# Performance work log

Measured on AMD Instinct MI355X. Metric: run time of the kernel, lower is better.

## Reference

```python
import jax, jax.numpy as jnp
import numpy as np

B, C, H, W = 16, 256, 32, 32
DIM = H * W  # LayerNorm/Linear dim == h*w per the rearrange in forward


def _conv1x1(x, w, b):
    # x: [b,c,h,w], w: [out,in] (1x1 kernel squeezed), b: [out]
    return jnp.einsum('bchw,oc->bohw', x, w) + b[None, :, None, None]


def _layernorm(x, g, b, eps=1e-5):
    mu = jnp.mean(x, axis=-1, keepdims=True)
    var = jnp.var(x, axis=-1, keepdims=True)
    return (x - mu) / jnp.sqrt(var + eps) * g + b


def setup_inputs() -> dict:
    key = jax.random.key(0)
    ks = jax.random.split(key, 12)
    n = jax.random.normal
    k_cdc = (2.0 / (2 * C)) ** 0.5   # kaiming_normal fan_in = 2C
    k_v = (2.0 / C) ** 0.5           # fan_in = C
    k_lin = (2.0 / DIM) ** 0.5       # fan_in = DIM
    return {
        'x_spa': n(ks[0], (B, C, H, W), jnp.float32),
        'x_freq': n(ks[1], (B, C, H, W), jnp.float32),
        'w_cdc': n(ks[2], (C, 2 * C), jnp.float32) * k_cdc,
        'b_cdc': jnp.zeros((C,), jnp.float32),
        'w_sv': n(ks[3], (C, C), jnp.float32) * k_v,
        'b_sv': jnp.zeros((C,), jnp.float32),
        'w_fv': n(ks[4], (C, C), jnp.float32) * k_v,
        'b_fv': jnp.zeros((C,), jnp.float32),
        'ln_w': jnp.ones((DIM,), jnp.float32),
        'ln_b': jnp.zeros((DIM,), jnp.float32),
        'w_qk': n(ks[5], (2 * DIM, DIM), jnp.float32) * k_lin,  # Linear(dim, 2*dim), no bias
        'w_spa': n(ks[6], (DIM, DIM), jnp.float32) * k_lin,
        'b_spa': jnp.zeros((DIM,), jnp.float32),
        'w_frq': n(ks[7], (DIM, DIM), jnp.float32) * k_lin,
        'b_frq': jnp.zeros((DIM,), jnp.float32),
    }


def reference(x_spa, x_freq, w_cdc, b_cdc, w_sv, b_sv, w_fv, b_fv,
              ln_w, ln_b, w_qk, w_spa, b_spa, w_frq, b_frq):
    b, c, h, w = x_spa.shape
    hw = h * w
    scale = hw ** (-0.5)
    v_spa = _conv1x1(x_spa, w_sv, b_sv).reshape(b, c, hw)
    v_freq = _conv1x1(x_freq, w_fv, b_fv).reshape(b, c, hw)
    x = _conv1x1(jnp.concatenate([x_spa, x_freq], axis=1), w_cdc, b_cdc).reshape(b, c, hw)
    x = _layernorm(x, ln_w, ln_b)
    qk = x @ w_qk.T                       # [b, c, 2*hw]
    q, k = jnp.split(qk, 2, axis=-1)      # each [b, c, hw]
    att = jnp.einsum('bcn,bcm->bnm', q, k) * scale   # q^T k over channels: [b, hw, hw]
    att_spa = jax.nn.softmax(att @ w_spa.T + b_spa, axis=-1)
    att_frq = jax.nn.softmax(att @ w_frq.T + b_frq, axis=-1)
    out_spa = x_spa + jnp.einsum('bcn,bnm->bcm', v_spa, att_spa).reshape(b, c, h, w)
    out_freq = x_freq + jnp.einsum('bcn,bnm->bcm', v_freq, att_frq).reshape(b, c, h, w)
    return out_spa, out_freq
```

## Files before the change

kernel.cpp:

```cpp
#include <hip/hip_runtime.h>
#include <hip/hip_bf16.h>

typedef __hip_bfloat16 bf16;
typedef __attribute__((ext_vector_type(8))) short bf16x8v;
typedef __attribute__((ext_vector_type(4))) float f32x4v;

__device__ __forceinline__ float bfbits2f(unsigned short h) {
    union { unsigned int u; float f; } v; v.u = ((unsigned int)h) << 16; return v.f;
}
__device__ __forceinline__ unsigned short f2bfbits(float f) {
    bf16 h = __float2bfloat16(f);
    unsigned short s;
    __builtin_memcpy(&s, &h, 2);
    return s;
}
__device__ __forceinline__ float load1_any(const void* p, long idx, bool f32) {
    if (f32) return ((const float*)p)[idx];
    return bfbits2f(((const unsigned short*)p)[idx]);
}
__device__ __forceinline__ float4 loadbf4(const bf16* p) {
    ushort4 u = *reinterpret_cast<const ushort4*>(p);
    return make_float4(bfbits2f(u.x), bfbits2f(u.y), bfbits2f(u.z), bfbits2f(u.w));
}
__device__ __forceinline__ void store_bf4(bf16* p, float a, float b, float c, float d) {
    ushort4 o;
    o.x = f2bfbits(a); o.y = f2bfbits(b); o.z = f2bfbits(c); o.w = f2bfbits(d);
    *reinterpret_cast<ushort4*>(p) = o;
}
__device__ __forceinline__ void gl16(const void* g, void* l) {
    __builtin_amdgcn_global_load_lds(
        (const __attribute__((address_space(1))) unsigned int*)g,
        (__attribute__((address_space(3))) unsigned int*)l, 16, 0, 0);
}

__global__ __launch_bounds__(1024)
void detect_kernel(const unsigned short* __restrict__ x, int* __restrict__ flag) {
    const int tid = threadIdx.x;
    int zc = 0, hc = 0;
    const uint4* xv = (const uint4*)x;
#pragma unroll
    for (int p = 0; p < 16; ++p) {
        uint4 v = xv[p * 1024 + tid];
        unsigned s0 = v.x & 0xFFFFu, s1 = v.y & 0xFFFFu;
        unsigned s2 = v.z & 0xFFFFu, s3 = v.w & 0xFFFFu;
        zc += (int)(s0 == 0) + (int)(s1 == 0) + (int)(s2 == 0) + (int)(s3 == 0);
        hc += (int)(((s0 >> 7) & 0xFFu) >= 0x90u) + (int)(((s1 >> 7) & 0xFFu) >= 0x90u)
            + (int)(((s2 >> 7) & 0xFFu) >= 0x90u) + (int)(((s3 >> 7) & 0xFFu) >= 0x90u);
    }
#pragma unroll
    for (int off = 32; off > 0; off >>= 1) {
        zc += __shfl_down(zc, off);
        hc += __shfl_down(hc, off);
    }
    __shared__ int rz[16], rh[16];
    if ((tid & 63) == 0) { rz[tid >> 6] = zc; rh[tid >> 6] = hc; }
    __syncthreads();
    if (tid == 0) {
        int Z = 0, H = 0;
#pragma unroll
        for (int i = 0; i < 16; ++i) { Z += rz[i]; H += rh[i]; }
        *flag = (Z > 60000 || H > 256) ? 1 : 0;
    }
}

__global__ void diag_kernel(float* __restrict__ out, float val) {
    if (threadIdx.x == 0) out[0] = val;
}

__global__ __launch_bounds__(256)
void convert6_kernel(const void* __restrict__ s0, const void* __restrict__ s1,
                     const void* __restrict__ s2, const void* __restrict__ s3,
                     const void* __restrict__ s4, const void* __restrict__ s5,
                     bf16* __restrict__ dst, const int* __restrict__ dflag) {
    const bool f32 = (*dflag != 0);
    for (long i = (long)blockIdx.x * 256 + threadIdx.x; i < 4456448;
         i += (long)gridDim.x * 256) {
        const void* s; long o;
        if (i < 131072)       { s = s0; o = i; }
        else if (i < 196608)  { s = s1; o = i - 131072; }
        else if (i < 262144)  { s = s2; o = i - 196608; }
        else if (i < 2359296) { s = s3; o = i - 262144; }
        else if (i < 3407872) { s = s4; o = i - 2359296; }
        else                  { s = s5; o = i - 3407872; }
        dst[i] = __float2bfloat16(load1_any(s, o, f32));
    }
}

__global__ __launch_bounds__(256)
void xpose_conv_kernel(const void* __restrict__ x1, const void* __restrict__ x2,
                       bf16* __restrict__ dst, int bofs, int zsplit,
                       const int* __restrict__ dflag) {
    const bool f32 = (*dflag != 0);
    __shared__ float t[64][65];
    const int ch0 = blockIdx.y * 64, n0 = blockIdx.x * 64, z = blockIdx.z;
    const bool hiz = (z >= zsplit);
    const int zl = hiz ? z - zsplit : z;
    const void* x = hiz ? x2 : x1;
    const long sb = (long)(zl + bofs) * 262144, db = (long)z * 262144;
    const int tid = threadIdx.x;
#pragma unroll
    for (int p = 0; p < 16; ++p) {
        int e = tid + p * 256; int sch = e >> 6, sn = e & 63;
        t[sch][sn] = load1_any(x, sb + (long)(ch0 + sch) * 1024 + n0 + sn, f32);
    }
    __syncthreads();
#pragma unroll
    for (int p = 0; p < 16; ++p) {
        int e = tid + p * 256; int dn = e >> 6, dch = e & 63;
        dst[db + (long)(n0 + dn) * 256 + ch0 + dch] = __float2bfloat16(t[dch][dn]);
    }
}

__global__ __launch_bounds__(256)
void smnorm_kernel(bf16* __restrict__ X, float* __restrict__ invS) {
    const int tid = threadIdx.x;
    const int cg = tid & 7;
    const int js = tid >> 3;
    const int n0 = blockIdx.x * 64;
    const long zb = (long)blockIdx.y * 1048576;
    unsigned short* Xp = (unsigned short*)X + zb + n0 + cg * 8;

    float m[8];
#pragma unroll
    for (int q = 0; q < 8; ++q) m[q] = -3.4e38f;
#pragma unroll 4
    for (int r = 0; r < 32; ++r) {
        bf16x8v u = *(const bf16x8v*)(Xp + (long)(js * 32 + r) * 1024);
#pragma unroll
        for (int q = 0; q < 8; ++q)
            m[q] = fmaxf(m[q], bfbits2f((unsigned short)u[q]));
    }
    __shared__ float sh[32][8][8];
    __shared__ float Mc[64];
#pragma unroll
    for (int q = 0; q < 8; ++q) sh[js][cg][q] = m[q];
    __syncthreads();
    if (tid < 64) {
        float mm = -3.4e38f;
#pragma unroll 8
        for (int s = 0; s < 32; ++s) mm = fmaxf(mm, sh[s][tid >> 3][tid & 7]);
        Mc[tid] = mm;
    }
    __syncthreads();
    float M8[8], s8[8];
#pragma unroll
    for (int q = 0; q < 8; ++q) { M8[q] = Mc[cg * 8 + q]; s8[q] = 0.f; }
#pragma unroll 4
    for (int r = 0; r < 32; ++r) {
        long off = (long)(js * 32 + r) * 1024;
        bf16x8v u = *(const bf16x8v*)(Xp + off);
        bf16x8v o;
#pragma unroll
        for (int q = 0; q < 8; ++q) {
            float e = __expf(bfbits2f((unsigned short)u[q]) - M8[q]);
            s8[q] += e;
            o[q] = (short)f2bfbits(e);
        }
        *(bf16x8v*)(Xp + off) = o;
    }
    __syncthreads();
#pragma unroll
    for (int q = 0; q < 8; ++q) sh[js][cg][q] = s8[q];
    __syncthreads();
    if (tid < 64) {
        float ss = 0.f;
#pragma unroll 8
        for (int s = 0; s < 32; ++s) ss += sh[s][tid >> 3][tid & 7];
        invS[(long)blockIdx.y * 1024 + n0 + tid] = 1.0f / ss;
    }
}

template <int EPI>
__global__ __launch_bounds__(256)
void mfma_nt(const bf16* __restrict__ A1, const bf16* __restrict__ A2,
             long aB1, long aB2, int ldA1, int ldA2,
             const bf16* __restrict__ B1, const bf16* __restrict__ B2,
             long bB1, long bB2, int ldB1, int ldB2,
             int ksplit, long kOff2,
             void* __restrict__ out1, void* __restrict__ out2,
             long oB1, long oB2, int ldO1, int ldO2,
             int K, float scale,
             const void* __restrict__ bias1, const void* __restrict__ bias2,
             const void* __restrict__ res1, const void* __restrict__ res2,
             long rBatch, int bofs, int zsplit, int swapXY,
             const int* __restrict__ dflag) {
    __shared__ short As[5][4096];
    __shared__ short Bs[5][4096];
    const int tid  = threadIdx.x;
    const int lane = tid & 63, wave = tid >> 6;
    const int quad = lane >> 4, lrow = lane & 15;
    const int wm = (wave >> 1) * 64, wn = (wave & 1) * 64;
    const int z  = blockIdx.z;
    const bool hiz = (z >= zsplit);
    const int zl = hiz ? z - zsplit : z;
    const bool sw = hiz && swapXY;
    const int n0 = (sw ? blockIdx.y : blockIdx.x) * 128;
    const int m0 = (sw ? blockIdx.x : blockIdx.y) * 128;
    const int ldA = hiz ? ldA2 : ldA1, ldB = hiz ? ldB2 : ldB1;
    const int ldO = hiz ? ldO2 : ldO1;
    const int srow = tid >> 2, sseg = tid & 3;
    const int sl = sseg ^ ((srow >> 1) & 3);
    const int xq = quad ^ ((lrow >> 1) & 3);

    const bf16* Ab = (hiz ? A2 : A1) + (long)zl * (hiz ? aB2 : aB1);
    const bf16* Bb = (hiz ? B2 : B1) + (long)zl * (hiz ? bB2 : bB1);

    auto stage = [&](int buf, int k0) {
        const bf16* asrc = Ab + (long)k0;
        const bf16* bsrc = Bb + ((k0 < ksplit) ? (long)k0 : (long)(k0 - ksplit) + kOff2);
        const bf16* ga0 = asrc + (long)(m0 + srow) * ldA + sl * 8;
        const bf16* ga1 = asrc + (long)(m0 + 64 + srow) * ldA + sl * 8;
        const bf16* gb0 = bsrc + (long)(n0 + srow) * ldB + sl * 8;
        const bf16* gb1 = bsrc + (long)(n0 + 64 + srow) * ldB + sl * 8;
        short* la = &As[buf][wave * 512];
        short* lb = &Bs[buf][wave * 512];
        gl16(ga0, la);
        gl16(ga1, la + 2048);
        gl16(gb0, lb);
        gl16(gb1, lb + 2048);
    };

    f32x4v acc[4][4] = {};
    const int nt = K >> 5;
    stage(0, 0);
    if (nt > 1) stage(1, 32);
    if (nt > 2) stage(2, 64);
    if (nt > 3) stage(3, 96);

    int cur = 0;
    for (int t = 0; t < nt; ++t) {
        const int rem = nt - 1 - t;
        if (rem >= 3)      asm volatile("s_waitcnt vmcnt(12)" ::: "memory");
        else if (rem == 2) asm volatile("s_waitcnt vmcnt(8)" ::: "memory");
        else if (rem == 1) asm volatile("s_waitcnt vmcnt(4)" ::: "memory");
        else               asm volatile("s_waitcnt vmcnt(0)" ::: "memory");
        __builtin_amdgcn_s_barrier();
        __builtin_amdgcn_sched_barrier(0);
        bf16x8v bfr[4], afr[4];
#pragma unroll
        for (int j = 0; j < 4; ++j)
            bfr[j] = *(const bf16x8v*)&Bs[cur][(wn + j * 16 + lrow) * 32 + xq * 8];
#pragma unroll
        for (int i = 0; i < 4; ++i)
            afr[i] = *(const bf16x8v*)&As[cur][(wm + i * 16 + lrow) * 32 + xq * 8];
        asm volatile("s_waitcnt lgkmcnt(0)" ::: "memory");
        __builtin_amdgcn_sched_barrier(0);
        if (t + 4 < nt) {
            int nb = cur + 4; if (nb >= 5) nb -= 5;
            stage(nb, (t + 4) << 5);
        }
#pragma unroll
        for (int i = 0; i < 4; ++i)
#pragma unroll
            for (int j = 0; j < 4; ++j)
                acc[i][j] = __builtin_amdgcn_mfma_f32_16x16x32_bf16(afr[i], bfr[j], acc[i][j], 0, 0, 0);
        cur = (cur == 4) ? 0 : cur + 1;
    }

    const bool f32 = (*dflag != 0);
    const void* bias = hiz ? bias2 : bias1;
    if (EPI != 3) {
        bf16* O = (bf16*)(hiz ? out2 : out1) + (long)zl * (hiz ? oB2 : oB1);
        const float* csp = (EPI == 4)
            ? (const float*)(hiz ? res2 : res1) + (long)zl * rBatch : nullptr;
#pragma unroll
        for (int i = 0; i < 4; ++i) {
            int row0 = m0 + wm + i * 16 + quad * 4;
            float rb[4] = {0.f, 0.f, 0.f, 0.f};
            if (EPI == 1 || EPI == 2 || EPI == 4) {
#pragma unroll
                for (int r = 0; r < 4; ++r) rb[r] = load1_any(bias, row0 + r, f32);
            }
#pragma unroll
            for (int j = 0; j < 4; ++j) {
                int col = n0 + wn + j * 16 + lrow;
                float cs = (EPI == 4) ? csp[col] : 1.0f;
#pragma unroll
                for (int r = 0; r < 4; ++r) {
                    float vv = acc[i][j][r];
                    if (EPI == 1) vv += rb[r];
                    if (EPI == 2) vv = vv * scale + rb[r];
                    if (EPI == 4) vv = (vv + rb[r]) * cs;
                    O[(long)(row0 + r) * ldO + col] = __float2bfloat16(vv);
                }
            }
        }
    } else {
        float* O = (float*)(hiz ? out2 : out1);
        const void* res = hiz ? res2 : res1;
        const long ob  = (long)(zl + bofs) * (hiz ? oB2 : oB1);
        const long rbb = (long)(zl + bofs) * rBatch;
#pragma unroll
        for (int i = 0; i < 4; ++i) {
            int row0 = m0 + wm + i * 16 + quad * 4;
#pragma unroll
            for (int j = 0; j < 4; ++j) {
                int col = n0 + wn + j * 16 + lrow;
#pragma unroll
                for (int r = 0; r < 4; ++r) {
                    float rv = load1_any(res, rbb + (long)(row0 + r) * ldO + col, f32);
                    O[ob + (long)(row0 + r) * ldO + col] = acc[i][j][r] + rv;
                }
            }
        }
    }
}

__global__ __launch_bounds__(256)
void layernorm_kernel(bf16* __restrict__ x, const void* __restrict__ g,
                      const void* __restrict__ beta, const int* __restrict__ dflag) {
    const bool f32 = (*dflag != 0);
    bf16* p = x + (long)blockIdx.x * 1024;
    const int tid = threadIdx.x;
    float4 v = loadbf4(p + tid * 4);
    float s  = v.x + v.y + v.z + v.w;
    float ss = v.x * v.x + v.y * v.y + v.z * v.z + v.w * v.w;
#pragma unroll
    for (int off = 32; off > 0; off >>= 1) {
        s  += __shfl_down(s, off);
        ss += __shfl_down(ss, off);
    }
    __shared__ float sh[8];
    __shared__ float sh_mu, sh_rs;
    if ((tid & 63) == 0) { sh[tid >> 6] = s; sh[4 + (tid >> 6)] = ss; }
    __syncthreads();
    if (tid == 0) {
        float S  = sh[0] + sh[1] + sh[2] + sh[3];
        float SS = sh[4] + sh[5] + sh[6] + sh[7];
        float mu = S * (1.0f / 1024.0f);
        float var = SS * (1.0f / 1024.0f) - mu * mu;
        sh_mu = mu;
        sh_rs = rsqrtf(fmaxf(var, 0.0f) + 1e-5f);
    }
    __syncthreads();
    float mu = sh_mu, rs = sh_rs;
    float gx = load1_any(g, tid * 4 + 0, f32), gy = load1_any(g, tid * 4 + 1, f32);
    float gz = load1_any(g, tid * 4 + 2, f32), gw = load1_any(g, tid * 4 + 3, f32);
    float bx = load1_any(beta, tid * 4 + 0, f32), by = load1_any(beta, tid * 4 + 1, f32);
    float bz = load1_any(beta, tid * 4 + 2, f32), bw = load1_any(beta, tid * 4 + 3, f32);
    store_bf4(p + tid * 4,
              (v.x - mu) * rs * gx + bx, (v.y - mu) * rs * gy + by,
              (v.z - mu) * rs * gz + bz, (v.w - mu) * rs * gw + bw);
}

extern "C" void kernel_launch(void* const* d_in, const int* in_sizes, int n_in,
                              void* d_out, int out_size, void* d_ws, size_t ws_size,
                              hipStream_t stream) {
    const void* x_spa  = d_in[0];
    const void* x_freq = d_in[1];
    const void* w_cdc  = d_in[2];
    const void* b_cdc  = d_in[3];
    const void* w_sv   = d_in[4];
    const void* b_sv   = d_in[5];
    const void* w_fv   = d_in[6];
    const void* b_fv   = d_in[7];
    const void* ln_w   = d_in[8];
    const void* ln_b   = d_in[9];
    const void* w_qk   = d_in[10];
    const void* w_spa  = d_in[11];
    const void* b_spa  = d_in[12];
    const void* w_frq  = d_in[13];
    const void* b_frq  = d_in[14];
    float* out = (float*)d_out;

    const int B = 16, C = 256;
    const long XB = 262144;
    const long PB = 1048576;

    int*  dflag = (int*)d_ws;
    bf16* wb    = (bf16*)((char*)d_ws + 4096);
    bf16* w_cdc_b = wb;
    bf16* w_sv_b  = w_cdc_b + 131072;
    bf16* w_fv_b  = w_sv_b  + 65536;
    bf16* w_qk_b  = w_fv_b  + 65536;
    bf16* w_spa_b = w_qk_b  + 2097152;
    bf16* w_frq_b = w_spa_b + 1048576;
    bf16* pb      = w_frq_b + 1048576;

    const size_t fixedB = 4096 + 4456448ull * 2;
    const size_t perB   = 8921088ull;
    size_t avail = (ws_size > fixedB) ? (ws_size - fixedB) : 0;
    long gmax = (long)(avail / perB);
    const bool wsOK = (gmax >= 1);
    int G = wsOK ? (int)(gmax > 16 ? 16 : gmax) : 1;

    bf16* xT    = pb;
    bf16* xln   = xT   + 2L * G * XB;
    bf16* kb    = xln  + (long)G * XB;
    bf16* qT    = kb   + (long)G * XB;
    bf16* TT    = qT   + (long)G * XB;
    bf16* vb    = TT   + 2L * G * XB;
    bf16* attpT = vb   + 2L * G * XB;
    float* invS = (float*)(attpT + 2L * G * PB);

    dim3 blk(256);
    detect_kernel<<<dim3(1), dim3(1024), 0, stream>>>((const unsigned short*)x_spa, dflag);

    if (!wsOK) {
        float mb = (float)(ws_size >> 20);
        diag_kernel<<<dim3(1), dim3(64), 0, stream>>>(out, 1000.0f * (mb + 1.0f));
        return;
    }

    convert6_kernel<<<dim3(4352), blk, 0, stream>>>(w_cdc, w_sv, w_fv, w_qk, w_spa, w_frq,
                                                    wb, dflag);

    for (int b0 = 0; b0 < B; b0 += G) {
        int g = (B - b0 < G) ? (B - b0) : G;

        xpose_conv_kernel<<<dim3(16, 4, 2 * g), blk, 0, stream>>>(
            x_spa, x_freq, xT, b0, g, dflag);

        mfma_nt<1><<<dim3(8, 2, g), blk, 0, stream>>>(
            w_cdc_b, w_cdc_b, 0, 0, 512, 512,
            xT, xT, XB, XB, 256, 256, 256, (long)g * XB,
            xln, xln, XB, XB, 1024, 1024,
            512, 1.0f, b_cdc, b_cdc, nullptr, nullptr, 0, 0, g, 0, dflag);
        layernorm_kernel<<<dim3(g * C), blk, 0, stream>>>(xln, ln_w, ln_b, dflag);

        mfma_nt<0><<<dim3(8, 2, 2 * g), blk, 0, stream>>>(
            xln, w_qk_b, XB, 0, 1024, 1024,
            w_qk_b + 1048576, xln, 0, XB, 1024, 1024, 1024, 0,
            kb, qT, XB, XB, 1024, 256,
            1024, 1.0f, nullptr, nullptr, nullptr, nullptr, 0, 0, g, 1, dflag);

        mfma_nt<0><<<dim3(2, 8, 2 * g), blk, 0, stream>>>(
            w_spa_b, w_frq_b, 0, 0, 1024, 1024,
            kb, kb, XB, XB, 1024, 1024, 1024, 0,
            TT, TT + (long)g * XB, XB, XB, 256, 256,
            1024, 1.0f, nullptr, nullptr, nullptr, nullptr, 0, 0, g, 0, dflag);

        mfma_nt<2><<<dim3(8, 8, 2 * g), blk, 0, stream>>>(
            TT, TT + (long)g * XB, XB, XB, 256, 256,
            qT, qT, XB, XB, 256, 256, 256, 0,
            attpT, attpT + (long)g * PB, PB, PB, 1024, 1024,
            256, 0.03125f, b_spa, b_frq, nullptr, nullptr, 0, 0, g, 0, dflag);

        smnorm_kernel<<<dim3(16, 2 * g), blk, 0, stream>>>(attpT, invS);

        mfma_nt<4><<<dim3(8, 2, 2 * g), blk, 0, stream>>>(
            w_sv_b, w_fv_b, 0, 0, 256, 256,
            xT, xT + (long)g * XB, XB, XB, 256, 256, 256, 0,
            vb, vb + (long)g * XB, XB, XB, 1024, 1024,
            256, 1.0f, b_sv, b_fv, invS, invS + (long)g * 1024, 1024, 0, g, 0, dflag);

        mfma_nt<3><<<dim3(8, 2, 2 * g), blk, 0, stream>>>(
            vb, vb + (long)g * XB, XB, XB, 1024, 1024,
            attpT, attpT + (long)g * PB, PB, PB, 1024, 1024, 1024, 0,
            out, out + 4194304, XB, XB, 1024, 1024,
            1024, 1.0f, nullptr, nullptr, x_spa, x_freq, XB, b0, g, 0, dflag);
    }
}
```

Before: 346.5 us.

## Precompute fused Wspa·Wk weights, batch GEMMs across samples, add 512-thread MFMA kernel

Precomputes W_spa·W_k^T (and W_frq) once per call through a transposed copy of the k-half of w_qk. This folds the k-projection into the attention-logit GEMM chain, so the per-batch k GEMM and the T=Wspa·k GEMM become a single GEMM on the layernormed activations. Activations are relaid out so several GEMMs treat the batch as one wide N dimension. A new 512-thread MFMA kernel with 128x256 or 256x256 tiles is used for the large GEMMs, and setprio is raised around the MFMA blocks. This adds workspace and a per-call weight-fusion GEMM, and the changed association order may shift bf16 rounding.

```diff
diff --git a/kernel.cpp b/kernel.cpp
--- a/kernel.cpp
+++ b/kernel.cpp
@@ -83,6 +83,24 @@
         else if (i < 3407872) { s = s4; o = i - 2359296; }
         else                  { s = s5; o = i - 3407872; }
         dst[i] = __float2bfloat16(load1_any(s, o, f32));
+    }
+}
+
+__global__ __launch_bounds__(256)
+void xpose_w_kernel(const bf16* __restrict__ src, bf16* __restrict__ dst) {
+    __shared__ float t[64][65];
+    const int c0 = blockIdx.x * 64, r0 = blockIdx.y * 64;
+    const int tid = threadIdx.x;
+#pragma unroll
+    for (int p = 0; p < 16; ++p) {
+        int e = tid + p * 256; int r = e >> 6, c = e & 63;
+        t[r][c] = __bfloat162float(src[(long)(r0 + r) * 1024 + c0 + c]);
+    }
+    __syncthreads();
+#pragma unroll
+    for (int p = 0; p < 16; ++p) {
+        int e = tid + p * 256; int r = e >> 6, c = e & 63;
+        dst[(long)(c0 + r) * 1024 + r0 + c] = __float2bfloat16(t[c][r]);
     }
 }
 
@@ -208,16 +226,10 @@
     auto stage = [&](int buf, int k0) {
         const bf16* asrc = Ab + (long)k0;
         const bf16* bsrc = Bb + ((k0 < ksplit) ? (long)k0 : (long)(k0 - ksplit) + kOff2);
-        const bf16* ga0 = asrc + (long)(m0 + srow) * ldA + sl * 8;
-        const bf16* ga1 = asrc + (long)(m0 + 64 + srow) * ldA + sl * 8;
-        const bf16* gb0 = bsrc + (long)(n0 + srow) * ldB + sl * 8;
-        const bf16* gb1 = bsrc + (long)(n0 + 64 + srow) * ldB + sl * 8;
-        short* la = &As[buf][wave * 512];
-        short* lb = &Bs[buf][wave * 512];
-        gl16(ga0, la);
-        gl16(ga1, la + 2048);
-        gl16(gb0, lb);
-        gl16(gb1, lb + 2048);
+        gl16(asrc + (long)(m0 + srow) * ldA + sl * 8, &As[buf][wave * 512]);
+        gl16(asrc + (long)(m0 + 64 + srow) * ldA + sl * 8, &As[buf][2048 + wave * 512]);
+        gl16(bsrc + (long)(n0 + srow) * ldB + sl * 8, &Bs[buf][wave * 512]);
+        gl16(bsrc + (long)(n0 + 64 + srow) * ldB + sl * 8, &Bs[buf][2048 + wave * 512]);
     };
 
     f32x4v acc[4][4] = {};
@@ -249,11 +261,13 @@
             int nb = cur + 4; if (nb >= 5) nb -= 5;
             stage(nb, (t + 4) << 5);
         }
+        __builtin_amdgcn_s_setprio(1);
 #pragma unroll
         for (int i = 0; i < 4; ++i)
 #pragma unroll
             for (int j = 0; j < 4; ++j)
                 acc[i][j] = __builtin_amdgcn_mfma_f32_16x16x32_bf16(afr[i], bfr[j], acc[i][j], 0, 0, 0);
+        __builtin_amdgcn_s_setprio(0);
         cur = (cur == 4) ? 0 : cur + 1;
     }
 
@@ -306,11 +320,150 @@
     }
 }
 
+template <int BM, int EPI>
+__global__ __launch_bounds__(512, 2)
+void mfma_nt2(const bf16* __restrict__ A1, const bf16* __restrict__ A2,
+              long aB, int ldA,
+              const bf16* __restrict__ B1, const bf16* __restrict__ B2,
+              long bB, int ldB,
+              void* __restrict__ out1, void* __restrict__ out2,
+              long oB, int ldO, int K, float scale,
+              const void* __restrict__ bias1, const void* __restrict__ bias2,
+              const void* __restrict__ res1, const void* __restrict__ res2,
+              long rBatch, int bofs, int zsplit,
+              const int* __restrict__ dflag) {
+    constexpr int NBUF = (BM == 128) ? 5 : 4;
+    constexpr int MI = BM / 32;
+    __shared__ short As[NBUF][BM * 32];
+    __shared__ short Bs[NBUF][8192];
+    const int tid  = threadIdx.x;
+    const int lane = tid & 63, wave = tid >> 6;
+    const int quad = lane >> 4, lrow = lane & 15;
+    const int wm = (wave >> 2) * (BM / 2), wn = (wave & 3) * 64;
+    const int n0 = blockIdx.x * 256, m0 = blockIdx.y * BM;
+    const int z  = blockIdx.z;
+    const bool hiz = (z >= zsplit);
+    const int zl = hiz ? z - zsplit : z;
+    const int srow = tid >> 2, sseg = tid & 3;
+    const int sl = sseg ^ ((srow >> 1) & 3);
+    const int xq = quad ^ ((lrow >> 1) & 3);
+
+    const bf16* Ab = (hiz ? A2 : A1) + (long)zl * aB;
+    const bf16* Bb = (hiz ? B2 : B1) + (long)zl * bB;
+
+    auto stage = [&](int buf, int k0) {
+        const bf16* asrc = Ab + (long)k0;
+        const bf16* bsrc = Bb + (long)k0;
+        gl16(asrc + (long)(m0 + srow) * ldA + sl * 8, &As[buf][wave * 512]);
+        if (BM == 256)
+            gl16(asrc + (long)(m0 + 128 + srow) * ldA + sl * 8, &As[buf][4096 + wave * 512]);
+        gl16(bsrc + (long)(n0 + srow) * ldB + sl * 8, &Bs[buf][wave * 512]);
+        gl16(bsrc + (long)(n0 + 128 + srow) * ldB + sl * 8, &Bs[buf][4096 + wave * 512]);
+    };
+
+    f32x4v acc[MI][4] = {};
+    const int nt = K >> 5;
+    stage(0, 0);
+    if (nt > 1) stage(1, 32);
+    if (nt > 2) stage(2, 64);
+    if (NBUF == 5 && nt > 3) stage(3, 96);
+
+    int cur = 0;
+    for (int t = 0; t < nt; ++t) {
+        const int rem = nt - 1 - t;
+        if (NBUF == 5) {
+            if (rem >= 3)      asm volatile("s_waitcnt vmcnt(9)" ::: "memory");
+            else if (rem == 2) asm volatile("s_waitcnt vmcnt(6)" ::: "memory");
+            else if (rem == 1) asm volatile("s_waitcnt vmcnt(3)" ::: "memory");
+            else               asm volatile("s_waitcnt vmcnt(0)" ::: "memory");
+        } else {
+            if (rem >= 2)      asm volatile("s_waitcnt vmcnt(8)" ::: "memory");
+            else if (rem == 1) asm volatile("s_waitcnt vmcnt(4)" ::: "memory");
+            else               asm volatile("s_waitcnt vmcnt(0)" ::: "memory");
+        }
+        __builtin_amdgcn_s_barrier();
+        __builtin_amdgcn_sched_barrier(0);
+        bf16x8v bfr[4], afr[MI];
+#pragma unroll
+        for (int j = 0; j < 4; ++j)
+            bfr[j] = *(const bf16x8v*)&Bs[cur][(wn + j * 16 + lrow) * 32 + xq * 8];
+#pragma unroll
+        for (int i = 0; i < MI; ++i)
+            afr[i] = *(const bf16x8v*)&As[cur][(wm + i * 16 + lrow) * 32 + xq * 8];
+        asm volatile("s_waitcnt lgkmcnt(0)" ::: "memory");
+        __builtin_amdgcn_sched_barrier(0);
+        if (t + NBUF - 1 < nt) {
+            int nb = cur + NBUF - 1; if (nb >= NBUF) nb -= NBUF;
+            stage(nb, (t + NBUF - 1) << 5);
+        }
+        __builtin_amdgcn_s_setprio(1);
+#pragma unroll
+        for (int i = 0; i < MI; ++i)
+#pragma unroll
+            for (int j = 0; j < 4; ++j)
+                acc[i][j] = __builtin_amdgcn_mfma_f32_16x16x32_bf16(afr[i], bfr[j], acc[i][j], 0, 0, 0);
+        __builtin_amdgcn_s_setprio(0);
+        cur = (cur + 1 == NBUF) ? 0 : cur + 1;
+    }
+
+    const bool f32 = (*dflag != 0);
+    const void* bias = hiz ? bias2 : bias1;
+    if (EPI != 3) {
+        bf16* O = (bf16*)(hiz ? out2 : out1) + (long)zl * oB;
+        const float* csp = (EPI == 4)
+            ? (const float*)(hiz ? res2 : res1) + (long)zl * rBatch : nullptr;
+#pragma unroll
+        for (int i = 0; i < MI; ++i) {
+            int row0 = m0 + wm + i * 16 + quad * 4;
+            float rb[4] = {0.f, 0.f, 0.f, 0.f};
+            if (EPI == 1 || EPI == 2 || EPI == 4) {
+#pragma unroll
+                for (int r = 0; r < 4; ++r) rb[r] = load1_any(bias, row0 + r, f32);
+            }
+#pragma unroll
+            for (int j = 0; j < 4; ++j) {
+                int col = n0 + wn + j * 16 + lrow;
+                float cs = (EPI == 4) ? csp[col] : 1.0f;
+#pragma unroll
+                for (int r = 0; r < 4; ++r) {
+                    float vv = acc[i][j][r];
+                    if (EPI == 1) vv += rb[r];
+                    if (EPI == 2) vv = vv * scale + rb[r];
+                    if (EPI == 4) vv = (vv + rb[r]) * cs;
+                    O[(long)(row0 + r) * ldO + col] = __float2bfloat16(vv);
+                }
+            }
+        }
+    } else {
+        float* O = (float*)(hiz ? out2 : out1);
+        const void* res = hiz ? res2 : res1;
+        const long ob  = (long)(zl + bofs) * oB;
+        const long rbb = (long)(zl + bofs) * rBatch;
+#pragma unroll
+        for (int i = 0; i < MI; ++i) {
+            int row0 = m0 + wm + i * 16 + quad * 4;
+#pragma unroll
+            for (int j = 0; j < 4; ++j) {
+                int col = n0 + wn + j * 16 + lrow;
+#pragma unroll
+                for (int r = 0; r < 4; ++r) {
+                    float rv = load1_any(res, rbb + (long)(row0 + r) * ldO + col, f32);
+                    O[ob + (long)(row0 + r) * ldO + col] = acc[i][j][r] + rv;
+                }
+            }
+        }
+    }
+}
+
 __global__ __launch_bounds__(256)
-void layernorm_kernel(bf16* __restrict__ x, const void* __restrict__ g,
-                      const void* __restrict__ beta, const int* __restrict__ dflag) {
+void layernorm_kernel(const bf16* __restrict__ src, bf16* __restrict__ dst,
+                      const void* __restrict__ g, const void* __restrict__ beta,
+                      int gN, const int* __restrict__ dflag) {
     const bool f32 = (*dflag != 0);
-    bf16* p = x + (long)blockIdx.x * 1024;
+    const int zc = blockIdx.x;
+    const int zz = zc >> 8, c = zc & 255;
+    const bf16* p = src + (long)c * gN + (long)zz * 1024;
+    bf16* q = dst + (long)zc * 1024;
     const int tid = threadIdx.x;
     float4 v = loadbf4(p + tid * 4);
     float s  = v.x + v.y + v.z + v.w;
@@ -338,7 +491,7 @@
     float gz = load1_any(g, tid * 4 + 2, f32), gw = load1_any(g, tid * 4 + 3, f32);
     float bx = load1_any(beta, tid * 4 + 0, f32), by = load1_any(beta, tid * 4 + 1, f32);
     float bz = load1_any(beta, tid * 4 + 2, f32), bw = load1_any(beta, tid * 4 + 3, f32);
-    store_bf4(p + tid * 4,
+    store_bf4(q + tid * 4,
               (v.x - mu) * rs * gx + bx, (v.y - mu) * rs * gy + by,
               (v.z - mu) * rs * gz + bz, (v.w - mu) * rs * gw + bw);
 }
@@ -375,23 +528,26 @@
     bf16* w_qk_b  = w_fv_b  + 65536;
     bf16* w_spa_b = w_qk_b  + 2097152;
     bf16* w_frq_b = w_spa_b + 1048576;
-    bf16* pb      = w_frq_b + 1048576;
-
-    const size_t fixedB = 4096 + 4456448ull * 2;
+    bf16* w_qk_hiT= w_frq_b + 1048576;
+    bf16* W1s     = w_qk_hiT + 1048576;
+    bf16* W1f     = W1s + 1048576;
+    bf16* pb      = W1f + 1048576;
+
+    const size_t fixedB = 4096 + 7602176ull * 2;
     const size_t perB   = 8921088ull;
     size_t avail = (ws_size > fixedB) ? (ws_size - fixedB) : 0;
     long gmax = (long)(avail / perB);
     const bool wsOK = (gmax >= 1);
     int G = wsOK ? (int)(gmax > 16 ? 16 : gmax) : 1;
 
-    bf16* xT    = pb;
-    bf16* xln   = xT   + 2L * G * XB;
-    bf16* kb    = xln  + (long)G * XB;
-    bf16* qT    = kb   + (long)G * XB;
-    bf16* TT    = qT   + (long)G * XB;
-    bf16* vb    = TT   + 2L * G * XB;
-    bf16* attpT = vb   + 2L * G * XB;
-    float* invS = (float*)(attpT + 2L * G * PB);
+    bf16* xT     = pb;
+    bf16* xlnF   = xT   + 2L * G * XB;
+    bf16* xln2   = xlnF + (long)G * XB;
+    bf16* qT     = xln2 + (long)G * XB;
+    bf16* TT     = qT   + (long)G * XB;
+    bf16* vb     = TT   + 2L * G * XB;
+    bf16* attpT  = vb   + 2L * G * XB;
+    float* invS  = (float*)(attpT + 2L * G * PB);
 
     dim3 blk(256);
     detect_kernel<<<dim3(1), dim3(1024), 0, stream>>>((const unsigned short*)x_spa, dflag);
@@ -404,50 +560,57 @@
 
     convert6_kernel<<<dim3(4352), blk, 0, stream>>>(w_cdc, w_sv, w_fv, w_qk, w_spa, w_frq,
                                                     wb, dflag);
+    xpose_w_kernel<<<dim3(16, 16), blk, 0, stream>>>(w_qk_b + 1048576, w_qk_hiT);
+    mfma_nt<0><<<dim3(8, 8, 2), blk, 0, stream>>>(
+        w_spa_b, w_frq_b, 0, 0, 1024, 1024,
+        w_qk_hiT, w_qk_hiT, 0, 0, 1024, 1024, 1024, 0,
+        W1s, W1f, 0, 0, 1024, 1024,
+        1024, 1.0f, nullptr, nullptr, nullptr, nullptr, 0, 0, 1, 0, dflag);
 
     for (int b0 = 0; b0 < B; b0 += G) {
         int g = (B - b0 < G) ? (B - b0) : G;
+        const int gN = g * 1024;
 
         xpose_conv_kernel<<<dim3(16, 4, 2 * g), blk, 0, stream>>>(
             x_spa, x_freq, xT, b0, g, dflag);
 
-        mfma_nt<1><<<dim3(8, 2, g), blk, 0, stream>>>(
+        mfma_nt<1><<<dim3(8 * g, 2, 1), blk, 0, stream>>>(
             w_cdc_b, w_cdc_b, 0, 0, 512, 512,
-            xT, xT, XB, XB, 256, 256, 256, (long)g * XB,
-            xln, xln, XB, XB, 1024, 1024,
-            512, 1.0f, b_cdc, b_cdc, nullptr, nullptr, 0, 0, g, 0, dflag);
-        layernorm_kernel<<<dim3(g * C), blk, 0, stream>>>(xln, ln_w, ln_b, dflag);
-
-        mfma_nt<0><<<dim3(8, 2, 2 * g), blk, 0, stream>>>(
-            xln, w_qk_b, XB, 0, 1024, 1024,
-            w_qk_b + 1048576, xln, 0, XB, 1024, 1024, 1024, 0,
-            kb, qT, XB, XB, 1024, 256,
-            1024, 1.0f, nullptr, nullptr, nullptr, nullptr, 0, 0, g, 1, dflag);
-
-        mfma_nt<0><<<dim3(2, 8, 2 * g), blk, 0, stream>>>(
-            w_spa_b, w_frq_b, 0, 0, 1024, 1024,
-            kb, kb, XB, XB, 1024, 1024, 1024, 0,
-            TT, TT + (long)g * XB, XB, XB, 256, 256,
-            1024, 1.0f, nullptr, nullptr, nullptr, nullptr, 0, 0, g, 0, dflag);
-
-        mfma_nt<2><<<dim3(8, 8, 2 * g), blk, 0, stream>>>(
-            TT, TT + (long)g * XB, XB, XB, 256, 256,
-            qT, qT, XB, XB, 256, 256, 256, 0,
-            attpT, attpT + (long)g * PB, PB, PB, 1024, 1024,
-            256, 0.03125f, b_spa, b_frq, nullptr, nullptr, 0, 0, g, 0, dflag);
+            xT, xT, 0, 0, 256, 256, 256, (long)g * XB,
+            xlnF, xlnF, 0, 0, gN, gN,
+            512, 1.0f, b_cdc, b_cdc, nullptr, nullptr, 0, 0, 1, 0, dflag);
+        layernorm_kernel<<<dim3(g * C), blk, 0, stream>>>(xlnF, xln2, ln_w, ln_b, gN, dflag);
+
+        mfma_nt<0><<<dim3(2 * g, 8, 1), blk, 0, stream>>>(
+            w_qk_b, w_qk_b, 0, 0, 1024, 1024,
+            xln2, xln2, 0, 0, 1024, 1024, 1024, 0,
+            qT, qT, 0, 0, g * 256, g * 256,
+            1024, 1.0f, nullptr, nullptr, nullptr, nullptr, 0, 0, 1, 0, dflag);
+
+        mfma_nt2<128, 0><<<dim3(g, 8, 2), dim3(512), 0, stream>>>(
+            W1s, W1f, 0, 1024,
+            xln2, xln2, 0, 1024,
+            TT, TT + (long)1024 * g * 256, 0, g * 256,
+            1024, 1.0f, nullptr, nullptr, nullptr, nullptr, 0, 0, 1, dflag);
+
+        mfma_nt2<256, 2><<<dim3(4, 4, 2 * g), dim3(512), 0, stream>>>(
+            TT, TT + (long)1024 * g * 256, 256, g * 256,
+            qT, qT, 256, g * 256,
+            attpT, attpT + (long)g * PB, PB, 1024,
+            256, 0.03125f, b_spa, b_frq, nullptr, nullptr, 0, 0, g, dflag);
 
         smnorm_kernel<<<dim3(16, 2 * g), blk, 0, stream>>>(attpT, invS);
 
-        mfma_nt<4><<<dim3(8, 2, 2 * g), blk, 0, stream>>>(
-            w_sv_b, w_fv_b, 0, 0, 256, 256,
-            xT, xT + (long)g * XB, XB, XB, 256, 256, 256, 0,
-            vb, vb + (long)g * XB, XB, XB, 1024, 1024,
-            256, 1.0f, b_sv, b_fv, invS, invS + (long)g * 1024, 1024, 0, g, 0, dflag);
-
-        mfma_nt<3><<<dim3(8, 2, 2 * g), blk, 0, stream>>>(
-            vb, vb + (long)g * XB, XB, XB, 1024, 1024,
-            attpT, attpT + (long)g * PB, PB, PB, 1024, 1024, 1024, 0,
-            out, out + 4194304, XB, XB, 1024, 1024,
-            1024, 1.0f, nullptr, nullptr, x_spa, x_freq, XB, b0, g, 0, dflag);
-    }
-}
+        mfma_nt2<128, 4><<<dim3(4 * g, 2, 2), dim3(512), 0, stream>>>(
+            w_sv_b, w_fv_b, 0, 256,
+            xT, xT + (long)g * XB, 0, 256,
+            vb, vb + (long)256 * gN, 0, gN,
+            256, 1.0f, b_sv, b_fv, invS, invS + gN, 0, 0, 1, dflag);
+
+        mfma_nt2<128, 3><<<dim3(4, 2, 2 * g), dim3(512), 0, stream>>>(
+            vb, vb + (long)256 * gN, 1024, gN,
+            attpT, attpT + (long)g * PB, PB, 1024,
+            out, out + 4194304, XB, 1024,
+            1024, 1.0f, nullptr, nullptr, x_spa, x_freq, XB, b0, g, dflag);
+    }
+}
```

New measurement: 358.1 us. 3.3% more time.
